# Optimization experiments

Measured on AMD Instinct MI355X. Metric: run time of the kernel, lower is better.

Reference implementation:

```python
import jax, jax.numpy as jnp
import numpy as np

TAU = 2.0      # LIF time constant
VTH = 1.0      # spike threshold
ALPHA = 4.0    # sigmoid surrogate slope (spikingjelly default)
EPS = 1e-5     # BN eps

@jax.custom_vjp
def spike_fn(x):
    return (x >= 0.0).astype(x.dtype)

def _spike_fwd(x):
    return spike_fn(x), x

def _spike_bwd(x, g):
    s = jax.nn.sigmoid(ALPHA * x)
    return (g * ALPHA * s * (1.0 - s),)

spike_fn.defvjp(_spike_fwd, _spike_bwd)

def conv2d(x, w, stride=1):
    return jax.lax.conv_general_dilated(
        x, w, (stride, stride), 'SAME',
        dimension_numbers=('NCHW', 'OIHW', 'NCHW'))

def bn(x, g, b, m, v):
    # eval-mode BatchNorm2d over channel axis 1
    scale = g / jnp.sqrt(v + EPS)
    return (x - m[:, None, None]) * scale[:, None, None] + b[:, None, None]

def lif_step(v, x):
    # charge, fire, hard reset to 0 (detach_reset)
    v = v + (x - v) / TAU
    s = spike_fn(v - VTH)
    v = (1.0 - jax.lax.stop_gradient(s)) * v
    return v, s

def lif_multistep(x_seq):
    v0 = jnp.zeros_like(x_seq[0])
    _, s = jax.lax.scan(lif_step, v0, x_seq)
    return s

def setup_inputs():
    key = jax.random.key(0)
    ks = jax.random.split(key, 8)
    T, B, C, H, W = 4, 4, 2, 128, 128
    E = 256
    x = jax.random.normal(ks[0], (T, B, C, H, W), jnp.float32)
    w_proj = jax.random.normal(ks[1], (E // 2, C, 3, 3), jnp.float32) * 0.2
    w_temp = jax.random.normal(ks[2], (C, E // 2, 3, 3), jnp.float32) * 0.05
    w1 = jax.random.normal(ks[3], (E, E // 2, 3, 3), jnp.float32) * 0.03
    w_res = jax.random.normal(ks[4], (E, E // 2, 1, 1), jnp.float32) * 0.09
    def bn_params(k, c):
        kk = jax.random.split(k, 2)
        return (jnp.abs(jax.random.normal(kk[0], (c,), jnp.float32)) + 0.5,
                jax.random.normal(kk[1], (c,), jnp.float32) * 0.1,
                jnp.zeros((c,), jnp.float32), jnp.ones((c,), jnp.float32))
    g0, b0, m0, v0 = bn_params(ks[5], E // 2)
    gt, bt, mt, vt = bn_params(ks[6], C)
    g1, b1, m1, v1 = bn_params(ks[7], E)
    gr, br, mr, vr = bn_params(jax.random.fold_in(key, 99), E)
    return dict(x=x, w_proj=w_proj, g0=g0, b0=b0, m0=m0, v0=v0,
                w_temp=w_temp, gt=gt, bt=bt, mt=mt, vt=vt,
                w1=w1, g1=g1, b1=b1, m1=m1, v1=v1,
                w_res=w_res, gr=gr, br=br, mr=mr, vr=vr)

def reference(x, w_proj, g0, b0, m0, v0, w_temp, gt, bt, mt, vt,
              w1, g1, b1, m1, v1, w_res, gr, br, mr, vr):
    T, B, C, H, W = x.shape
    half = w_proj.shape[0]
    # stf_1 recurrent coding: x_in[t] = x[t] + x_out[t-1]; LIF states persist
    def step(carry, x_t):
        x_out, vp, vtm = carry
        x_in = x_t + x_out
        h = bn(conv2d(x_in, w_proj), g0, b0, m0, v0)          # [B,half,H,W]
        vp, s1 = lif_step(vp, h)                              # proj_lif
        y = bn(conv2d(s1, w_temp), gt, bt, mt, vt)            # [B,C,H,W]
        vtm, s2 = lif_step(vtm, y)                            # proj_temporal_lif
        return (s2, vp, vtm), s1
    init = (jnp.zeros((B, C, H, W), x.dtype),
            jnp.zeros((B, half, H, W), x.dtype),
            jnp.zeros((B, C, H, W), x.dtype))
    _, spikes = jax.lax.scan(step, init, x)                   # [T,B,half,H,W]
    xf = spikes.reshape(T * B, half, H, W)
    xa = bn(conv2d(xf, w1), g1, b1, m1, v1).reshape(T, B, -1, H, W)
    xa = lif_multistep(xa)                                    # proj1_lif
    xr = bn(conv2d(xf, w_res), gr, br, mr, vr).reshape(T, B, -1, H, W)
    xr = lif_multistep(xr)                                    # proj_res_lif
    return xa + xr
```

## Files before the change

### kernel.cpp

```cpp
#include <hip/hip_runtime.h>
#include <math.h>

#define HW 16384

typedef __attribute__((ext_vector_type(8))) _Float16 half8;
typedef __attribute__((ext_vector_type(4))) float f32x4;

__global__ __launch_bounds__(256)
void k_proj0r(const float* __restrict__ xt, const float* __restrict__ wp,
              const float* __restrict__ g0, const float* __restrict__ b0,
              const float* __restrict__ m0, const float* __restrict__ v0,
              float* __restrict__ vp, unsigned char* __restrict__ s1t,
              const float* __restrict__ w1, const float* __restrict__ wres,
              const float* __restrict__ g1, const float* __restrict__ b1,
              const float* __restrict__ m1, const float* __restrict__ v1,
              const float* __restrict__ gr, const float* __restrict__ br,
              const float* __restrict__ mr, const float* __restrict__ vr,
              short* __restrict__ whi, short* __restrict__ wmid,
              short* __restrict__ rhi, short* __restrict__ rmid,
              float* __restrict__ bias1, float* __restrict__ biasr) {
    const int tid = threadIdx.x;
    if (blockIdx.x >= 1024) {
        int i = (blockIdx.x - 1024) * 256 + tid;
        if (i < 294912) {
            int n = i / 1152, rem = i % 1152;
            int ic = rem / 9, tap = rem % 9;
            float sc = g1[n] / sqrtf(v1[n] + 1e-5f);
            float wv = (w1[i] * sc) * 4096.0f;
            _Float16 h = (_Float16)wv;
            float r1 = wv - (float)h;
            _Float16 m = (_Float16)r1;
            int kb = ic >> 5, q = (ic >> 3) & 3, j = ic & 7;
            size_t f = ((((size_t)(kb * 9 + tap)) * 4 + q) * 256 + n) * 8 + j;
            whi[f]  = __builtin_bit_cast(short, h);
            wmid[f] = __builtin_bit_cast(short, m);
        }
        if (i < 32768) {
            int n = i >> 7, ic = i & 127;
            float sc = gr[n] / sqrtf(vr[n] + 1e-5f);
            float wv = (wres[i] * sc) * 4096.0f;
            _Float16 h = (_Float16)wv;
            float r1 = wv - (float)h;
            _Float16 m = (_Float16)r1;
            int kb = ic >> 5, q = (ic >> 3) & 3, j = ic & 7;
            size_t f = (((size_t)kb * 4 + q) * 256 + n) * 8 + j;
            rhi[f]  = __builtin_bit_cast(short, h);
            rmid[f] = __builtin_bit_cast(short, m);
        }
        if (i < 256) {
            float sc1 = g1[i] / sqrtf(v1[i] + 1e-5f);
            bias1[i] = (b1[i] - m1[i] * sc1) * 4096.0f;
            float scr_ = gr[i] / sqrtf(vr[i] + 1e-5f);
            biasr[i] = (br[i] - mr[i] * scr_) * 4096.0f;
        }
        return;
    }

    __shared__ float xin[2 * 10 * 36];
    const int vt = blockIdx.x;
    const int bx = vt & 3, by = (vt >> 2) & 15, bz = vt >> 6;
    const int b   = bz >> 2;
    const int ocq = bz & 3;
    const int gy0 = by * 8, gx0 = bx * 32;

    for (int i = tid; i < 680; i += 256) {
        int ch = i / 340, rem = i % 340;
        int r = rem / 34, c = rem % 34;
        int gy = gy0 - 1 + r, gx = gx0 - 1 + c;
        float val = 0.f;
        if (gy >= 0 && gy < 128 && gx >= 0 && gx < 128) {
            int idx = ((b * 2 + ch) << 14) + (gy << 7) + gx;
            val = xt[idx];
        }
        xin[(ch * 10 + r) * 36 + c] = val;
    }
    __syncthreads();

    const int prow = tid >> 5, pcol = tid & 31;
    float xw[2][3][3];
#pragma unroll
    for (int ch = 0; ch < 2; ++ch)
#pragma unroll
        for (int ky = 0; ky < 3; ++ky)
#pragma unroll
            for (int kx = 0; kx < 3; ++kx)
                xw[ch][ky][kx] = xin[(ch * 10 + prow + ky) * 36 + pcol + kx];

    const int pix = ((gy0 + prow) << 7) + gx0 + pcol;
    const int oc_beg = ocq * 32;
    unsigned int pk = 0u;
#pragma unroll
    for (int oo = 0; oo < 32; ++oo) {
        const int oc = oc_beg + oo;
        float acc = 0.f;
#pragma unroll
        for (int ch = 0; ch < 2; ++ch)
#pragma unroll
            for (int ky = 0; ky < 3; ++ky)
#pragma unroll
                for (int kx = 0; kx < 3; ++kx)
                    acc = fmaf(wp[((oc * 2 + ch) * 3 + ky) * 3 + kx], xw[ch][ky][kx], acc);
        float sc = g0[oc] / sqrtf(v0[oc] + 1e-5f);
        float h  = (acc - m0[oc]) * sc + b0[oc];
        int idx = ((b * 128 + oc) << 14) + pix;
        float v = 0.f;
        v = v + (h - v) * 0.5f;
        bool s = (v >= 1.0f);
        vp[idx] = s ? 0.f : v;
        pk |= (s ? 1u : 0u) << oo;
    }
    *(unsigned int*)(s1t + ((((size_t)b << 14) + pix) << 4) + ocq * 4) = pk;
}

__global__ __launch_bounds__(256)
void k_proj(const float* __restrict__ xt, const float* __restrict__ xout,
            const float* __restrict__ wp,
            const float* __restrict__ g, const float* __restrict__ bb,
            const float* __restrict__ mm, const float* __restrict__ vv,
            float* __restrict__ vp, unsigned char* __restrict__ s1t,
            int last) {
    __shared__ float xin[2 * 10 * 36];
    const int tid = threadIdx.x;
    const int b   = blockIdx.z >> 2;
    const int ocq = blockIdx.z & 3;
    const int gy0 = blockIdx.y * 8, gx0 = blockIdx.x * 32;

    for (int i = tid; i < 680; i += 256) {
        int ch = i / 340, rem = i % 340;
        int r = rem / 34, c = rem % 34;
        int gy = gy0 - 1 + r, gx = gx0 - 1 + c;
        float val = 0.f;
        if (gy >= 0 && gy < 128 && gx >= 0 && gx < 128) {
            int idx = ((b * 2 + ch) << 14) + (gy << 7) + gx;
            val = xt[idx] + xout[idx];
        }
        xin[(ch * 10 + r) * 36 + c] = val;
    }
    __syncthreads();

    const int prow = tid >> 5, pcol = tid & 31;
    float xw[2][3][3];
#pragma unroll
    for (int ch = 0; ch < 2; ++ch)
#pragma unroll
        for (int ky = 0; ky < 3; ++ky)
#pragma unroll
            for (int kx = 0; kx < 3; ++kx)
                xw[ch][ky][kx] = xin[(ch * 10 + prow + ky) * 36 + pcol + kx];

    const int pix = ((gy0 + prow) << 7) + gx0 + pcol;
    const int oc_beg = ocq * 32;
    unsigned int pk = 0u;
#pragma unroll
    for (int oo = 0; oo < 32; ++oo) {
        const int oc = oc_beg + oo;
        float acc = 0.f;
#pragma unroll
        for (int ch = 0; ch < 2; ++ch)
#pragma unroll
            for (int ky = 0; ky < 3; ++ky)
#pragma unroll
                for (int kx = 0; kx < 3; ++kx)
                    acc = fmaf(wp[((oc * 2 + ch) * 3 + ky) * 3 + kx], xw[ch][ky][kx], acc);
        float sc = g[oc] / sqrtf(vv[oc] + 1e-5f);
        float h  = (acc - mm[oc]) * sc + bb[oc];
        int idx = ((b * 128 + oc) << 14) + pix;
        float v = vp[idx];
        v = v + (h - v) * 0.5f;
        bool s = (v >= 1.0f);
        if (!last) vp[idx] = s ? 0.f : v;
        pk |= (s ? 1u : 0u) << oo;
    }
    *(unsigned int*)(s1t + ((((size_t)b << 14) + pix) << 4) + ocq * 4) = pk;
}

__global__ __launch_bounds__(256)
void k_temp(const unsigned char* __restrict__ s1t, const float* __restrict__ wt,
            const float* __restrict__ g, const float* __restrict__ bb,
            const float* __restrict__ mm, const float* __restrict__ vv,
            float* __restrict__ vtm, float* __restrict__ xout,
            int first, int lastv) {
    __shared__ unsigned char sl[49152];
    __shared__ float wls[2304];
    __shared__ float red[256];
    const int tid = threadIdx.x;
    const int b   = blockIdx.y;
    const int y0  = blockIdx.x;

    for (int i = tid; i < 2304; i += 256) wls[i] = wt[i];

    for (int i = tid; i < 384; i += 256) {
        int r = i >> 7, px = i & 127;
        int gy = y0 - 1 + r;
        uint4 d = make_uint4(0u, 0u, 0u, 0u);
        if (gy >= 0 && gy < 128)
            d = *(const uint4*)(s1t + ((((size_t)b << 14) + (gy << 7) + px) << 4));
        unsigned int bs[4] = {d.x, d.y, d.z, d.w};
#pragma unroll
        for (int icb = 0; icb < 16; ++icb) {
            unsigned int v8 = (bs[icb >> 2] >> ((icb & 3) * 8)) & 0xFFu;
            unsigned int lo = (v8 & 1u) | ((v8 & 2u) << 7) | ((v8 & 4u) << 14) | ((v8 & 8u) << 21);
            unsigned int hi = ((v8 >> 4) & 1u) | ((v8 & 32u) << 3) | ((v8 & 64u) << 10) | ((v8 & 128u) << 17);
            *(uint2*)&sl[(((icb * 3) + r) * 128 + (px ^ (icb & 7))) * 8] = make_uint2(lo, hi);
        }
    }
    __syncthreads();

    const int x = tid & 127, hf = tid >> 7;
    float a0 = 0.f, a1 = 0.f;
#pragma unroll 1
    for (int ii = 0; ii < 8; ++ii) {
        const int icb = hf * 8 + ii;
        int sw = icb & 7;
        const float* w0 = &wls[icb * 72];
        const float* w1_ = &wls[1152 + icb * 72];
#pragma unroll
        for (int dy = 0; dy < 3; ++dy) {
#pragma unroll
            for (int dx = 0; dx < 3; ++dx) {
                int xx = x - 1 + dx;
                if (xx < 0 || xx > 127) continue;
                uint2 d = *(const uint2*)&sl[((icb * 3 + dy) * 128 + (xx ^ sw)) * 8];
                int tap = dy * 3 + dx;
#pragma unroll
                for (int j = 0; j < 4; ++j) {
                    float f0 = (float)((d.x >> (8 * j)) & 0xFFu);
                    float f1 = (float)((d.y >> (8 * j)) & 0xFFu);
                    a0 = fmaf(w0[j * 9 + tap],        f0, a0);
                    a0 = fmaf(w0[(4 + j) * 9 + tap],  f1, a0);
                    a1 = fmaf(w1_[j * 9 + tap],       f0, a1);
                    a1 = fmaf(w1_[(4 + j) * 9 + tap], f1, a1);
                }
            }
        }
    }
    if (hf) { red[x] = a0; red[128 + x] = a1; }
    __syncthreads();
    if (!hf) {
        a0 += red[x]; a1 += red[128 + x];
#pragma unroll
        for (int oc = 0; oc < 2; ++oc) {
            float acc = (oc == 0) ? a0 : a1;
            float sc = g[oc] / sqrtf(vv[oc] + 1e-5f);
            float yv = (acc - mm[oc]) * sc + bb[oc];
            int idx = ((b * 2 + oc) << 14) + (y0 << 7) + x;
            float v = first ? 0.f : vtm[idx];
            v = v + (yv - v) * 0.5f;
            bool s = (v >= 1.0f);
            if (!lastv) vtm[idx] = s ? 0.f : v;
            xout[idx] = s ? 1.0f : 0.f;
        }
    }
}

__global__ __launch_bounds__(256, 3)
void k_fused(const unsigned char* __restrict__ s1c,
             const short* __restrict__ whi, const short* __restrict__ wmid,
             const short* __restrict__ rhi, const short* __restrict__ rmid,
             const float* __restrict__ bias1, const float* __restrict__ biasr,
             float* __restrict__ out) {
    __shared__ __align__(16) unsigned char bl[8704];
    __shared__ __align__(16) unsigned char xp[34816];

    const int tid = threadIdx.x;
    const int oc0 = blockIdx.x * 64;
    const int yb = blockIdx.y;
    const int b = yb >> 8, ry = (yb >> 2) & 63, cx = yb & 3;
    const int gy0 = ry * 2, gx0 = cx * 32;

    const int w   = tid >> 6, l = tid & 63;
    const int q   = l >> 4,  ln = l & 15;
    const int woc = w >> 1,  wpx = w & 1;

    const size_t wofs = ((size_t)q * 256 + oc0 + woc * 32 + ln) * 8;

    int pb[2], po[2], eb[2];
#pragma unroll
    for (int nt = 0; nt < 2; ++nt) {
        int px = wpx * 32 + nt * 16 + ln;
        int prow = px >> 5, pcol = px & 31;
        pb[nt] = prow * 34 + pcol;
        po[nt] = ((gy0 + prow) << 7) + gx0 + pcol;
        eb[nt] = pb[nt] * 64 + q * 16;
    }

    for (int cc = tid; cc < 544; cc += 256) {
        int t = cc / 136, p = cc - t * 136;
        int r = p / 34, c = p - r * 34;
        int gy = gy0 - 1 + r, gx = gx0 - 1 + c;
        uint4 d = make_uint4(0u, 0u, 0u, 0u);
        if (gy >= 0 && gy < 128 && gx >= 0 && gx < 128)
            d = *(const uint4*)(s1c + (size_t)t * 1048576 +
                                ((((size_t)b << 14) + (gy << 7) + gx) << 4));
        *(uint4*)(bl + cc * 16) = d;
    }
    __syncthreads();

    const float ds_ = 0.000244140625f;

    unsigned int srb[4];
    {
        f32x4 brr[2];
#pragma unroll
        for (int mt2 = 0; mt2 < 2; ++mt2)
#pragma unroll
            for (int rg = 0; rg < 4; ++rg)
                brr[mt2][rg] = biasr[oc0 + woc * 32 + mt2 * 16 + q * 4 + rg];

        float vres[2][2][4];
#pragma unroll
        for (int nt = 0; nt < 2; ++nt)
#pragma unroll
            for (int mt2 = 0; mt2 < 2; ++mt2)
#pragma unroll
                for (int rg = 0; rg < 4; ++rg) vres[nt][mt2][rg] = 0.f;

#pragma unroll
        for (int t = 0; t < 4; ++t) {
            const unsigned char* blt = bl + t * 2176;
            f32x4 accr[2][2];
#pragma unroll
            for (int nt = 0; nt < 2; ++nt)
#pragma unroll
                for (int mt2 = 0; mt2 < 2; ++mt2) accr[nt][mt2] = brr[mt2];

#pragma unroll
            for (int kb = 0; kb < 4; ++kb) {
                half8 B4[2];
#pragma unroll
                for (int nt = 0; nt < 2; ++nt) {
                    unsigned int v8 = blt[(pb[nt] + 35) * 16 + kb * 4 + q];
                    uint4 pk;
                    pk.x = ((v8 & 1u)          | ((v8 & 2u)   << 15)) * 0x3C00u;
                    pk.y = (((v8 >> 2) & 1u)   | ((v8 & 8u)   << 13)) * 0x3C00u;
                    pk.z = (((v8 >> 4) & 1u)   | ((v8 & 32u)  << 11)) * 0x3C00u;
                    pk.w = (((v8 >> 6) & 1u)   | ((v8 & 128u) << 9 )) * 0x3C00u;
                    B4[nt] = __builtin_bit_cast(half8, pk);
                }
                half8 RH[2], RM[2];
#pragma unroll
                for (int mt2 = 0; mt2 < 2; ++mt2) {
                    RH[mt2] = *(const half8*)(rhi  + wofs + (size_t)kb * 8192 + mt2 * 128);
                    RM[mt2] = *(const half8*)(rmid + wofs + (size_t)kb * 8192 + mt2 * 128);
                }
#pragma unroll
                for (int nt = 0; nt < 2; ++nt)
#pragma unroll
                    for (int mt2 = 0; mt2 < 2; ++mt2) {
                        accr[nt][mt2] = __builtin_amdgcn_mfma_f32_16x16x32_f16(RH[mt2], B4[nt], accr[nt][mt2], 0, 0, 0);
                        accr[nt][mt2] = __builtin_amdgcn_mfma_f32_16x16x32_f16(RM[mt2], B4[nt], accr[nt][mt2], 0, 0, 0);
                    }
            }

            unsigned int sb = 0u;
#pragma unroll
            for (int nt = 0; nt < 2; ++nt)
#pragma unroll
                for (int mt2 = 0; mt2 < 2; ++mt2)
#pragma unroll
                    for (int rg = 0; rg < 4; ++rg) {
                        float hr = accr[nt][mt2][rg] * ds_;
                        float u = vres[nt][mt2][rg];
                        u = u + (hr - u) * 0.5f;
                        bool sr_ = (u >= 1.0f);
                        vres[nt][mt2][rg] = sr_ ? 0.f : u;
                        sb |= (sr_ ? 1u : 0u) << (mt2 * 8 + rg * 2 + nt);
                    }
            srb[t] = sb;
        }
    }

    f32x4 acc[4][2][2];
#pragma unroll
    for (int mt2 = 0; mt2 < 2; ++mt2)
#pragma unroll
        for (int rg = 0; rg < 4; ++rg) {
            float bv = bias1[oc0 + woc * 32 + mt2 * 16 + q * 4 + rg];
#pragma unroll
            for (int t = 0; t < 4; ++t)
#pragma unroll
                for (int nt = 0; nt < 2; ++nt) acc[t][nt][mt2][rg] = bv;
        }

    const short* bh = whi  + wofs;
    const short* bm = wmid + wofs;
#pragma unroll 1
    for (int kb = 0; kb < 4; ++kb) {
        if (kb) __syncthreads();
        for (int cc = tid; cc < 2176; cc += 256) {
            int r = cc >> 2, c = cc & 3;
            unsigned int dw = *(const unsigned int*)(bl + r * 16 + kb * 4);
            unsigned int x0 = dw >> (c * 8);
            uint4 o;
            o.x = ((x0 & 1u)          | ((x0 & 2u)   << 15)) * 0x3C00u;
            o.y = (((x0 >> 2) & 1u)   | ((x0 & 8u)   << 13)) * 0x3C00u;
            o.z = (((x0 >> 4) & 1u)   | ((x0 & 32u)  << 11)) * 0x3C00u;
            o.w = (((x0 >> 6) & 1u)   | ((x0 & 128u) << 9 )) * 0x3C00u;
            *(uint4*)(xp + cc * 16) = o;
        }
        __syncthreads();

#pragma unroll
        for (int tap = 0; tap < 9; ++tap) {
            const int toff = ((tap / 3) * 34 + (tap % 3)) * 64;
            half8 AH[2], AM[2];
#pragma unroll
            for (int mt2 = 0; mt2 < 2; ++mt2) {
                AH[mt2] = *(const half8*)(bh + mt2 * 128);
                AM[mt2] = *(const half8*)(bm + mt2 * 128);
            }
#pragma unroll
            for (int t = 0; t < 4; ++t) {
                half8 B4[2];
#pragma unroll
                for (int nt = 0; nt < 2; ++nt)
                    B4[nt] = *(const half8*)(xp + t * 8704 + eb[nt] + toff);
#pragma unroll
                for (int nt = 0; nt < 2; ++nt)
#pragma unroll
                    for (int mt2 = 0; mt2 < 2; ++mt2) {
                        acc[t][nt][mt2] = __builtin_amdgcn_mfma_f32_16x16x32_f16(AH[mt2], B4[nt], acc[t][nt][mt2], 0, 0, 0);
                        acc[t][nt][mt2] = __builtin_amdgcn_mfma_f32_16x16x32_f16(AM[mt2], B4[nt], acc[t][nt][mt2], 0, 0, 0);
                    }
            }
            bh += 8192; bm += 8192;
        }
    }

    float va[2][2][4];
#pragma unroll
    for (int nt = 0; nt < 2; ++nt)
#pragma unroll
        for (int mt2 = 0; mt2 < 2; ++mt2)
#pragma unroll
            for (int rg = 0; rg < 4; ++rg) va[nt][mt2][rg] = 0.f;

#pragma unroll
    for (int t = 0; t < 4; ++t) {
        const size_t tb = ((size_t)((t * 4 + b) * 256 + oc0)) << 14;
#pragma unroll
        for (int mt2 = 0; mt2 < 2; ++mt2)
#pragma unroll
            for (int rg = 0; rg < 4; ++rg) {
                const size_t ob = tb + ((size_t)(woc * 32 + mt2 * 16 + q * 4 + rg) << 14);
#pragma unroll
                for (int nt = 0; nt < 2; ++nt) {
                    float ha = acc[t][nt][mt2][rg] * ds_;
                    float v = va[nt][mt2][rg];
                    v = v + (ha - v) * 0.5f;
                    bool s = (v >= 1.0f);
                    va[nt][mt2][rg] = s ? 0.f : v;
                    float sa = s ? 1.f : 0.f;
                    float sr = ((srb[t] >> (mt2 * 8 + rg * 2 + nt)) & 1u) ? 1.f : 0.f;
                    out[ob + po[nt]] = sa + sr;
                }
            }
    }
}

extern "C" void kernel_launch(void* const* d_in, const int* in_sizes, int n_in,
                              void* d_out, int out_size, void* d_ws, size_t ws_size,
                              hipStream_t stream) {
    const float* x      = (const float*)d_in[0];
    const float* w_proj = (const float*)d_in[1];
    const float* g0 = (const float*)d_in[2];
    const float* b0 = (const float*)d_in[3];
    const float* m0 = (const float*)d_in[4];
    const float* v0 = (const float*)d_in[5];
    const float* w_temp = (const float*)d_in[6];
    const float* gt = (const float*)d_in[7];
    const float* bt = (const float*)d_in[8];
    const float* mt = (const float*)d_in[9];
    const float* vt = (const float*)d_in[10];
    const float* w1 = (const float*)d_in[11];
    const float* g1 = (const float*)d_in[12];
    const float* b1 = (const float*)d_in[13];
    const float* m1 = (const float*)d_in[14];
    const float* v1 = (const float*)d_in[15];
    const float* w_res = (const float*)d_in[16];
    const float* gr = (const float*)d_in[17];
    const float* br = (const float*)d_in[18];
    const float* mr = (const float*)d_in[19];
    const float* vr = (const float*)d_in[20];

    char* ws = (char*)d_ws;
    unsigned char* s1c = (unsigned char*)ws;
    float* vp    = (float*)(ws + 4194304);
    float* vtm   = (float*)(ws + 37748736);
    float* xout  = (float*)(ws + 38273024);
    short* whi   = (short*)(ws + 38797312);
    short* wmid  = (short*)(ws + 39387136);
    short* rhi   = (short*)(ws + 39976960);
    short* rmid  = (short*)(ws + 40042496);
    float* bias1 = (float*)(ws + 40108032);
    float* biasr = (float*)(ws + 40109056);

    k_proj0r<<<dim3(2176), dim3(256), 0, stream>>>(
        x, w_proj, g0, b0, m0, v0, vp, s1c,
        w1, w_res, g1, b1, m1, v1, gr, br, mr, vr,
        whi, wmid, rhi, rmid, bias1, biasr);

    k_temp<<<dim3(128, 4), dim3(256), 0, stream>>>(
        s1c, w_temp, gt, bt, mt, vt, vtm, xout, 1, 0);

    for (int t = 1; t < 4; ++t) {
        const float* xt = x + (size_t)t * 131072;
        unsigned char* s1t = s1c + (size_t)t * 1048576;
        k_proj<<<dim3(4, 16, 16), dim3(256), 0, stream>>>(
            xt, xout, w_proj, g0, b0, m0, v0, vp, s1t, t == 3);
        if (t < 3)
            k_temp<<<dim3(128, 4), dim3(256), 0, stream>>>(
                s1t, w_temp, gt, bt, mt, vt, vtm, xout, 0, t == 2);
    }

    k_fused<<<dim3(4, 1024), dim3(256), 0, stream>>>(
        s1c, whi, wmid, rhi, rmid, bias1, biasr, (float*)d_out);
}
```

Measured before the change: 626.4 us.

## Double-buffer spike expansion in fused conv and stage proj weights in LDS

The fused conv kernel now splits each K block into two time-pair phases and expands the next phase's packed spikes into a second LDS buffer while the MFMAs of the current phase run. This is meant to overlap the bit-to-fp16 expansion with tensor work and to leave only one barrier per phase. The accumulator is now indexed by a runtime-dependent time index inside an unroll-1 loop, which risks register spills or select chains. The projection kernels also copy conv weights and precomputed BN scale, mean and bias into shared memory, replacing what were probably uniform scalar global loads.

```diff
diff --git a/kernel.cpp b/kernel.cpp
--- a/kernel.cpp
+++ b/kernel.cpp
@@ -57,6 +57,8 @@
     }
 
     __shared__ float xin[2 * 10 * 36];
+    __shared__ float wls[2304];
+    __shared__ float bnsc[32], bnm[32], bnb[32];
     const int vt = blockIdx.x;
     const int bx = vt & 3, by = (vt >> 2) & 15, bz = vt >> 6;
     const int b   = bz >> 2;
@@ -74,6 +76,13 @@
         }
         xin[(ch * 10 + r) * 36 + c] = val;
     }
+    for (int i = tid; i < 2304; i += 256) wls[i] = wp[i];
+    if (tid < 32) {
+        int oc = ocq * 32 + tid;
+        bnsc[tid] = g0[oc] / sqrtf(v0[oc] + 1e-5f);
+        bnm[tid]  = m0[oc];
+        bnb[tid]  = b0[oc];
+    }
     __syncthreads();
 
     const int prow = tid >> 5, pcol = tid & 31;
@@ -99,9 +108,9 @@
             for (int ky = 0; ky < 3; ++ky)
 #pragma unroll
                 for (int kx = 0; kx < 3; ++kx)
-                    acc = fmaf(wp[((oc * 2 + ch) * 3 + ky) * 3 + kx], xw[ch][ky][kx], acc);
-        float sc = g0[oc] / sqrtf(v0[oc] + 1e-5f);
-        float h  = (acc - m0[oc]) * sc + b0[oc];
+                    acc = fmaf(wls[((oc * 2 + ch) * 3 + ky) * 3 + kx], xw[ch][ky][kx], acc);
+        float sc = bnsc[oo];
+        float h  = (acc - bnm[oo]) * sc + bnb[oo];
         int idx = ((b * 128 + oc) << 14) + pix;
         float v = 0.f;
         v = v + (h - v) * 0.5f;
@@ -120,6 +129,8 @@
             float* __restrict__ vp, unsigned char* __restrict__ s1t,
             int last) {
     __shared__ float xin[2 * 10 * 36];
+    __shared__ float wls[2304];
+    __shared__ float bnsc[32], bnm[32], bnb[32];
     const int tid = threadIdx.x;
     const int b   = blockIdx.z >> 2;
     const int ocq = blockIdx.z & 3;
@@ -136,6 +147,13 @@
         }
         xin[(ch * 10 + r) * 36 + c] = val;
     }
+    for (int i = tid; i < 2304; i += 256) wls[i] = wp[i];
+    if (tid < 32) {
+        int oc = ocq * 32 + tid;
+        bnsc[tid] = g[oc] / sqrtf(vv[oc] + 1e-5f);
+        bnm[tid]  = mm[oc];
+        bnb[tid]  = bb[oc];
+    }
     __syncthreads();
 
     const int prow = tid >> 5, pcol = tid & 31;
@@ -161,9 +179,9 @@
             for (int ky = 0; ky < 3; ++ky)
 #pragma unroll
                 for (int kx = 0; kx < 3; ++kx)
-                    acc = fmaf(wp[((oc * 2 + ch) * 3 + ky) * 3 + kx], xw[ch][ky][kx], acc);
-        float sc = g[oc] / sqrtf(vv[oc] + 1e-5f);
-        float h  = (acc - mm[oc]) * sc + bb[oc];
+                    acc = fmaf(wls[((oc * 2 + ch) * 3 + ky) * 3 + kx], xw[ch][ky][kx], acc);
+        float sc = bnsc[oo];
+        float h  = (acc - bnm[oo]) * sc + bnb[oo];
         int idx = ((b * 128 + oc) << 14) + pix;
         float v = vp[idx];
         v = v + (h - v) * 0.5f;
@@ -260,7 +278,7 @@
              const float* __restrict__ bias1, const float* __restrict__ biasr,
              float* __restrict__ out) {
     __shared__ __align__(16) unsigned char bl[8704];
-    __shared__ __align__(16) unsigned char xp[34816];
+    __shared__ __align__(16) unsigned char xp[2][17408];
 
     const int tid = threadIdx.x;
     const int oc0 = blockIdx.x * 64;
@@ -382,39 +400,47 @@
                 for (int nt = 0; nt < 2; ++nt) acc[t][nt][mt2][rg] = bv;
         }
 
-    const short* bh = whi  + wofs;
-    const short* bm = wmid + wofs;
+#define EXPAND(kb_, tp_, bf_)                                                  \
+    for (int cc = tid; cc < 1088; cc += 256) {                                 \
+        int r_ = cc >> 2, c_ = cc & 3;                                         \
+        unsigned int dw = *(const unsigned int*)(bl + ((tp_) * 272 + r_) * 16 + (kb_) * 4); \
+        unsigned int x0 = dw >> (c_ * 8);                                      \
+        uint4 o;                                                               \
+        o.x = ((x0 & 1u)          | ((x0 & 2u)   << 15)) * 0x3C00u;            \
+        o.y = (((x0 >> 2) & 1u)   | ((x0 & 8u)   << 13)) * 0x3C00u;            \
+        o.z = (((x0 >> 4) & 1u)   | ((x0 & 32u)  << 11)) * 0x3C00u;            \
+        o.w = (((x0 >> 6) & 1u)   | ((x0 & 128u) << 9 )) * 0x3C00u;            \
+        *(uint4*)(xp[bf_] + cc * 16) = o;                                      \
+    }
+
+    EXPAND(0, 0, 0);
+    __syncthreads();
+
 #pragma unroll 1
-    for (int kb = 0; kb < 4; ++kb) {
-        if (kb) __syncthreads();
-        for (int cc = tid; cc < 2176; cc += 256) {
-            int r = cc >> 2, c = cc & 3;
-            unsigned int dw = *(const unsigned int*)(bl + r * 16 + kb * 4);
-            unsigned int x0 = dw >> (c * 8);
-            uint4 o;
-            o.x = ((x0 & 1u)          | ((x0 & 2u)   << 15)) * 0x3C00u;
-            o.y = (((x0 >> 2) & 1u)   | ((x0 & 8u)   << 13)) * 0x3C00u;
-            o.z = (((x0 >> 4) & 1u)   | ((x0 & 32u)  << 11)) * 0x3C00u;
-            o.w = (((x0 >> 6) & 1u)   | ((x0 & 128u) << 9 )) * 0x3C00u;
-            *(uint4*)(xp + cc * 16) = o;
-        }
-        __syncthreads();
-
+    for (int p = 0; p < 8; ++p) {
+        const int kb = p >> 1, tp = p & 1, cur = p & 1;
+        if (p < 7) {
+            const int pn = p + 1;
+            EXPAND(pn >> 1, pn & 1, pn & 1);
+        }
+        const short* bhk = whi  + wofs + (size_t)kb * 73728;
+        const short* bmk = wmid + wofs + (size_t)kb * 73728;
 #pragma unroll
         for (int tap = 0; tap < 9; ++tap) {
             const int toff = ((tap / 3) * 34 + (tap % 3)) * 64;
             half8 AH[2], AM[2];
 #pragma unroll
             for (int mt2 = 0; mt2 < 2; ++mt2) {
-                AH[mt2] = *(const half8*)(bh + mt2 * 128);
-                AM[mt2] = *(const half8*)(bm + mt2 * 128);
+                AH[mt2] = *(const half8*)(bhk + tap * 8192 + mt2 * 128);
+                AM[mt2] = *(const half8*)(bmk + tap * 8192 + mt2 * 128);
             }
 #pragma unroll
-            for (int t = 0; t < 4; ++t) {
+            for (int tt = 0; tt < 2; ++tt) {
+                const int t = tp * 2 + tt;
                 half8 B4[2];
 #pragma unroll
                 for (int nt = 0; nt < 2; ++nt)
-                    B4[nt] = *(const half8*)(xp + t * 8704 + eb[nt] + toff);
+                    B4[nt] = *(const half8*)(xp[cur] + tt * 8704 + eb[nt] + toff);
 #pragma unroll
                 for (int nt = 0; nt < 2; ++nt)
 #pragma unroll
@@ -423,9 +449,10 @@
                         acc[t][nt][mt2] = __builtin_amdgcn_mfma_f32_16x16x32_f16(AM[mt2], B4[nt], acc[t][nt][mt2], 0, 0, 0);
                     }
             }
-            bh += 8192; bm += 8192;
-        }
-    }
+        }
+        __syncthreads();
+    }
+#undef EXPAND
 
     float va[2][2][4];
 #pragma unroll
```

Result: slower. 902.1 us (+44.0%).

## Widen fused conv tile to 128 output channels and stage proj weights in LDS

Applied to the files above, without the earlier changes.

The fused conv kernel now computes 128 output channels per block instead of 64, halving the grid in x. This halves the redundant spike unpacking into shared memory and the B-fragment loads per output, at the cost of twice as many accumulator registers and occupancy lowered to 2 blocks. The projection kernels also copy the conv weights and precomputed BN scale, mean and bias into shared memory, replacing repeated global/scalar loads and per-channel sqrt. Higher register pressure in the fused kernel could cause spills or lower latency hiding.

```diff
diff --git a/kernel.cpp b/kernel.cpp
--- a/kernel.cpp
+++ b/kernel.cpp
@@ -57,6 +57,8 @@
     }
 
     __shared__ float xin[2 * 10 * 36];
+    __shared__ float wls[2304];
+    __shared__ float bnsc[32], bnm[32], bnb[32];
     const int vt = blockIdx.x;
     const int bx = vt & 3, by = (vt >> 2) & 15, bz = vt >> 6;
     const int b   = bz >> 2;
@@ -74,6 +76,13 @@
         }
         xin[(ch * 10 + r) * 36 + c] = val;
     }
+    for (int i = tid; i < 2304; i += 256) wls[i] = wp[i];
+    if (tid < 32) {
+        int oc = ocq * 32 + tid;
+        bnsc[tid] = g0[oc] / sqrtf(v0[oc] + 1e-5f);
+        bnm[tid]  = m0[oc];
+        bnb[tid]  = b0[oc];
+    }
     __syncthreads();
 
     const int prow = tid >> 5, pcol = tid & 31;
@@ -99,9 +108,9 @@
             for (int ky = 0; ky < 3; ++ky)
 #pragma unroll
                 for (int kx = 0; kx < 3; ++kx)
-                    acc = fmaf(wp[((oc * 2 + ch) * 3 + ky) * 3 + kx], xw[ch][ky][kx], acc);
-        float sc = g0[oc] / sqrtf(v0[oc] + 1e-5f);
-        float h  = (acc - m0[oc]) * sc + b0[oc];
+                    acc = fmaf(wls[((oc * 2 + ch) * 3 + ky) * 3 + kx], xw[ch][ky][kx], acc);
+        float sc = bnsc[oo];
+        float h  = (acc - bnm[oo]) * sc + bnb[oo];
         int idx = ((b * 128 + oc) << 14) + pix;
         float v = 0.f;
         v = v + (h - v) * 0.5f;
@@ -120,6 +129,8 @@
             float* __restrict__ vp, unsigned char* __restrict__ s1t,
             int last) {
     __shared__ float xin[2 * 10 * 36];
+    __shared__ float wls[2304];
+    __shared__ float bnsc[32], bnm[32], bnb[32];
     const int tid = threadIdx.x;
     const int b   = blockIdx.z >> 2;
     const int ocq = blockIdx.z & 3;
@@ -136,6 +147,13 @@
         }
         xin[(ch * 10 + r) * 36 + c] = val;
     }
+    for (int i = tid; i < 2304; i += 256) wls[i] = wp[i];
+    if (tid < 32) {
+        int oc = ocq * 32 + tid;
+        bnsc[tid] = g[oc] / sqrtf(vv[oc] + 1e-5f);
+        bnm[tid]  = mm[oc];
+        bnb[tid]  = bb[oc];
+    }
     __syncthreads();
 
     const int prow = tid >> 5, pcol = tid & 31;
@@ -161,9 +179,9 @@
             for (int ky = 0; ky < 3; ++ky)
 #pragma unroll
                 for (int kx = 0; kx < 3; ++kx)
-                    acc = fmaf(wp[((oc * 2 + ch) * 3 + ky) * 3 + kx], xw[ch][ky][kx], acc);
-        float sc = g[oc] / sqrtf(vv[oc] + 1e-5f);
-        float h  = (acc - mm[oc]) * sc + bb[oc];
+                    acc = fmaf(wls[((oc * 2 + ch) * 3 + ky) * 3 + kx], xw[ch][ky][kx], acc);
+        float sc = bnsc[oo];
+        float h  = (acc - bnm[oo]) * sc + bnb[oo];
         int idx = ((b * 128 + oc) << 14) + pix;
         float v = vp[idx];
         v = v + (h - v) * 0.5f;
@@ -253,7 +271,7 @@
     }
 }
 
-__global__ __launch_bounds__(256, 3)
+__global__ __launch_bounds__(256, 2)
 void k_fused(const unsigned char* __restrict__ s1c,
              const short* __restrict__ whi, const short* __restrict__ wmid,
              const short* __restrict__ rhi, const short* __restrict__ rmid,
@@ -263,7 +281,7 @@
     __shared__ __align__(16) unsigned char xp[34816];
 
     const int tid = threadIdx.x;
-    const int oc0 = blockIdx.x * 64;
+    const int oc0 = blockIdx.x * 128;
     const int yb = blockIdx.y;
     const int b = yb >> 8, ry = (yb >> 2) & 63, cx = yb & 3;
     const int gy0 = ry * 2, gx0 = cx * 32;
@@ -272,7 +290,7 @@
     const int q   = l >> 4,  ln = l & 15;
     const int woc = w >> 1,  wpx = w & 1;
 
-    const size_t wofs = ((size_t)q * 256 + oc0 + woc * 32 + ln) * 8;
+    const size_t wofs = ((size_t)q * 256 + oc0 + woc * 64 + ln) * 8;
 
     int pb[2], po[2], eb[2];
 #pragma unroll
@@ -300,29 +318,29 @@
 
     unsigned int srb[4];
     {
-        f32x4 brr[2];
-#pragma unroll
-        for (int mt2 = 0; mt2 < 2; ++mt2)
+        f32x4 brr[4];
+#pragma unroll
+        for (int mt2 = 0; mt2 < 4; ++mt2)
 #pragma unroll
             for (int rg = 0; rg < 4; ++rg)
-                brr[mt2][rg] = biasr[oc0 + woc * 32 + mt2 * 16 + q * 4 + rg];
-
-        float vres[2][2][4];
+                brr[mt2][rg] = biasr[oc0 + woc * 64 + mt2 * 16 + q * 4 + rg];
+
+        float vres[2][4][4];
 #pragma unroll
         for (int nt = 0; nt < 2; ++nt)
 #pragma unroll
-            for (int mt2 = 0; mt2 < 2; ++mt2)
+            for (int mt2 = 0; mt2 < 4; ++mt2)
 #pragma unroll
                 for (int rg = 0; rg < 4; ++rg) vres[nt][mt2][rg] = 0.f;
 
 #pragma unroll
         for (int t = 0; t < 4; ++t) {
             const unsigned char* blt = bl + t * 2176;
-            f32x4 accr[2][2];
+            f32x4 accr[2][4];
 #pragma unroll
             for (int nt = 0; nt < 2; ++nt)
 #pragma unroll
-                for (int mt2 = 0; mt2 < 2; ++mt2) accr[nt][mt2] = brr[mt2];
+                for (int mt2 = 0; mt2 < 4; ++mt2) accr[nt][mt2] = brr[mt2];
 
 #pragma unroll
             for (int kb = 0; kb < 4; ++kb) {
@@ -337,16 +355,16 @@
                     pk.w = (((v8 >> 6) & 1u)   | ((v8 & 128u) << 9 )) * 0x3C00u;
                     B4[nt] = __builtin_bit_cast(half8, pk);
                 }
-                half8 RH[2], RM[2];
-#pragma unroll
-                for (int mt2 = 0; mt2 < 2; ++mt2) {
+                half8 RH[4], RM[4];
+#pragma unroll
+                for (int mt2 = 0; mt2 < 4; ++mt2) {
                     RH[mt2] = *(const half8*)(rhi  + wofs + (size_t)kb * 8192 + mt2 * 128);
                     RM[mt2] = *(const half8*)(rmid + wofs + (size_t)kb * 8192 + mt2 * 128);
                 }
 #pragma unroll
                 for (int nt = 0; nt < 2; ++nt)
 #pragma unroll
-                    for (int mt2 = 0; mt2 < 2; ++mt2) {
+                    for (int mt2 = 0; mt2 < 4; ++mt2) {
                         accr[nt][mt2] = __builtin_amdgcn_mfma_f32_16x16x32_f16(RH[mt2], B4[nt], accr[nt][mt2], 0, 0, 0);
                         accr[nt][mt2] = __builtin_amdgcn_mfma_f32_16x16x32_f16(RM[mt2], B4[nt], accr[nt][mt2], 0, 0, 0);
                     }
@@ -356,7 +374,7 @@
 #pragma unroll
             for (int nt = 0; nt < 2; ++nt)
 #pragma unroll
-                for (int mt2 = 0; mt2 < 2; ++mt2)
+                for (int mt2 = 0; mt2 < 4; ++mt2)
 #pragma unroll
                     for (int rg = 0; rg < 4; ++rg) {
                         float hr = accr[nt][mt2][rg] * ds_;
@@ -370,12 +388,12 @@
         }
     }
 
-    f32x4 acc[4][2][2];
-#pragma unroll
-    for (int mt2 = 0; mt2 < 2; ++mt2)
+    f32x4 acc[4][2][4];
+#pragma unroll
+    for (int mt2 = 0; mt2 < 4; ++mt2)
 #pragma unroll
         for (int rg = 0; rg < 4; ++rg) {
-            float bv = bias1[oc0 + woc * 32 + mt2 * 16 + q * 4 + rg];
+            float bv = bias1[oc0 + woc * 64 + mt2 * 16 + q * 4 + rg];
 #pragma unroll
             for (int t = 0; t < 4; ++t)
 #pragma unroll
@@ -403,9 +421,9 @@
 #pragma unroll
         for (int tap = 0; tap < 9; ++tap) {
             const int toff = ((tap / 3) * 34 + (tap % 3)) * 64;
-            half8 AH[2], AM[2];
-#pragma unroll
-            for (int mt2 = 0; mt2 < 2; ++mt2) {
+            half8 AH[4], AM[4];
+#pragma unroll
+            for (int mt2 = 0; mt2 < 4; ++mt2) {
                 AH[mt2] = *(const half8*)(bh + mt2 * 128);
                 AM[mt2] = *(const half8*)(bm + mt2 * 128);
             }
@@ -418,7 +436,7 @@
 #pragma unroll
                 for (int nt = 0; nt < 2; ++nt)
 #pragma unroll
-                    for (int mt2 = 0; mt2 < 2; ++mt2) {
+                    for (int mt2 = 0; mt2 < 4; ++mt2) {
                         acc[t][nt][mt2] = __builtin_amdgcn_mfma_f32_16x16x32_f16(AH[mt2], B4[nt], acc[t][nt][mt2], 0, 0, 0);
                         acc[t][nt][mt2] = __builtin_amdgcn_mfma_f32_16x16x32_f16(AM[mt2], B4[nt], acc[t][nt][mt2], 0, 0, 0);
                     }
@@ -427,11 +445,11 @@
         }
     }
 
-    float va[2][2][4];
+    float va[2][4][4];
 #pragma unroll
     for (int nt = 0; nt < 2; ++nt)
 #pragma unroll
-        for (int mt2 = 0; mt2 < 2; ++mt2)
+        for (int mt2 = 0; mt2 < 4; ++mt2)
 #pragma unroll
             for (int rg = 0; rg < 4; ++rg) va[nt][mt2][rg] = 0.f;
 
@@ -439,10 +457,10 @@
     for (int t = 0; t < 4; ++t) {
         const size_t tb = ((size_t)((t * 4 + b) * 256 + oc0)) << 14;
 #pragma unroll
-        for (int mt2 = 0; mt2 < 2; ++mt2)
+        for (int mt2 = 0; mt2 < 4; ++mt2)
 #pragma unroll
             for (int rg = 0; rg < 4; ++rg) {
-                const size_t ob = tb + ((size_t)(woc * 32 + mt2 * 16 + q * 4 + rg) << 14);
+                const size_t ob = tb + ((size_t)(woc * 64 + mt2 * 16 + q * 4 + rg) << 14);
 #pragma unroll
                 for (int nt = 0; nt < 2; ++nt) {
                     float ha = acc[t][nt][mt2][rg] * ds_;
@@ -513,6 +531,6 @@
                 s1t, w_temp, gt, bt, mt, vt, vtm, xout, 0, t == 2);
     }
 
-    k_fused<<<dim3(4, 1024), dim3(256), 0, stream>>>(
+    k_fused<<<dim3(2, 1024), dim3(256), 0, stream>>>(
         s1c, whi, wmid, rhi, rmid, bias1, biasr, (float*)d_out);
 }
```

Measured after the change: 673.5 us. 7.5% more time.
